# Kernel tuning notes

Hardware: AMD Instinct MI355X
Metric: run time of the kernel (lower is better)

The kernel has to match this reference:

```python
import jax, jax.numpy as jnp
import numpy as np

N, D, R, B, K = 16384, 300, 10, 1024, 64


def setup_inputs() -> dict:
    key = jax.random.key(0)
    ks = jax.random.split(key, 6)
    return {
        "node_feat_src": jax.random.normal(ks[0], (N, D), jnp.float32),
        "node_feat_tgt": jax.random.normal(ks[1], (N, D), jnp.float32),
        "srcs_index": jax.random.randint(ks[2], (B, K), 0, N),
        "tgts_index": jax.random.randint(ks[3], (B, K), 0, N),
        "src_vs": jax.random.normal(ks[4], (R, D), jnp.float32),
        "tgt_vs": jax.random.normal(ks[5], (R, D), jnp.float32),
    }


def _tower(h, vs):
    # Householder chain: h @ (I - v v^T / (v^T v)) == h - ((h v) / (v^T v)) v^T
    def step(h, v):
        coef = (h @ v) / (v @ v)  # [N]
        return h - coef[:, None] * v[None, :], None
    h, _ = jax.lax.scan(step, h, vs)
    return h


def _l2norm(x):
    # matches F.normalize(p=2, eps=1e-12) over the last dim
    n = jnp.linalg.norm(x, axis=-1, keepdims=True)
    return x / jnp.maximum(n, 1e-12)


def reference(node_feat_src, node_feat_tgt, srcs_index, tgts_index, src_vs, tgt_vs):
    src_h = _tower(node_feat_src, src_vs)  # [N, D]
    tgt_h = _tower(node_feat_tgt, tgt_vs)  # [N, D]

    pos_src = _l2norm(src_h[srcs_index[:, 0]])  # [B, D]
    pos_tgt = _l2norm(tgt_h[tgts_index[:, 0]])  # [B, D]
    src_list = _l2norm(src_h[srcs_index])       # [B, K, D]
    tgt_list = _l2norm(tgt_h[tgts_index])       # [B, K, D]

    sim_src2tgt = jnp.einsum('bd,bkd->bk', pos_src, tgt_list)  # [B, K]
    sim_tgt2src = jnp.einsum('bd,bkd->bk', pos_tgt, src_list)  # [B, K]

    # CSLS hubness penalties: mean of top-10 cross-domain cosine sims
    sim_matrix = _l2norm(src_h) @ _l2norm(tgt_h).T  # [N, N]
    rt = jnp.mean(jax.lax.top_k(sim_matrix, 10)[0], axis=1)    # [N]
    rs = jnp.mean(jax.lax.top_k(sim_matrix.T, 10)[0], axis=1)  # [N]

    srcs_rt = rt[srcs_index]  # [B, K]
    tgts_rs = rs[tgts_index]  # [B, K]

    logits_src2tgt = sim_src2tgt * 2 - srcs_rt[:, 0:1] - tgts_rs
    logits_tgt2src = sim_tgt2src * 2 - tgts_rs[:, 0:1] - srcs_rt
    return logits_src2tgt, logits_tgt2src
```

## Files before the change

kernel.cpp:

```cpp
#include <hip/hip_runtime.h>
#include <hip/hip_bf16.h>

#define NN 16384
#define DD 300
#define DP 320
#define RR 10
#define BB 1024
#define KK 64
#define CAP 128
#define CAPL 512

typedef __attribute__((ext_vector_type(8))) short s8v;
typedef __attribute__((ext_vector_type(4))) float f4v;
typedef _Float16 h2 __attribute__((ext_vector_type(2)));

__device__ __forceinline__ unsigned mono2(unsigned d) {
    unsigned s = ((d >> 15) & 0x10001u) * 0xFFFFu;
    return d ^ (s | 0x80008000u);
}
__device__ __forceinline__ float key2f16(unsigned k) {
    unsigned short b = (k & 0x8000u) ? (unsigned short)(k ^ 0x8000u)
                                     : (unsigned short)(~k & 0xFFFFu);
    _Float16 hv = __builtin_bit_cast(_Float16, b);
    return (float)hv;
}

__device__ __forceinline__ h2 h2max(h2 a, h2 b) {
    return __builtin_elementwise_max(a, b);
}
__device__ __forceinline__ h2 hmax2s(h2 a, int xb) {
    int x = __shfl_xor(__builtin_bit_cast(int, a), xb);
    return h2max(a, __builtin_bit_cast(h2, x));
}
__device__ __forceinline__ h2 packh2(float a, float b) {
    h2 r; r[0] = (_Float16)a; r[1] = (_Float16)b; return r;
}

__device__ __forceinline__ void ins10(unsigned (&lst)[10], unsigned v) {
    #pragma unroll
    for (int q = 0; q < 10; ++q) {
        unsigned a  = lst[q];
        unsigned mx = a > v ? a : v;
        v           = a > v ? v : a;
        lst[q] = mx;
    }
}
__device__ __forceinline__ void ins10f(float (&lst)[10], float v) {
    #pragma unroll
    for (int q = 0; q < 10; ++q) {
        float a  = lst[q];
        float mx = fmaxf(a, v);
        v        = fminf(a, v);
        lst[q] = mx;
    }
}

__device__ __forceinline__ void xcd_map(int bid, int& by, int& bx) {
    const int xcd = bid & 7;
    const int s   = bid >> 3;
    bx = (xcd << 2) | (s & 3);
    by = s >> 2;
}

__device__ __forceinline__ void gload_lds16(const void* g, void* l) {
#if __has_builtin(__builtin_amdgcn_global_load_lds)
    __builtin_amdgcn_global_load_lds(
        (const __attribute__((address_space(1))) void*)g,
        (__attribute__((address_space(3))) void*)l, 16, 0, 0);
#else
    const int lane = threadIdx.x & 63;
    int4 v = *reinterpret_cast<const int4*>(g);
    *reinterpret_cast<int4*>((char*)l + lane * 16) = v;
#endif
}

__device__ __forceinline__ void stage_tile(
        const __hip_bfloat16* __restrict__ Ab, const __hip_bfloat16* __restrict__ Bb,
        int kb, char* lds, int w, int lane) {
    const int r8 = lane >> 3;
    const int u  = (lane & 7) ^ r8;
    const int row = w * 8 + r8;
    const size_t go = (size_t)row * DP + kb * 64 + u * 8;
    gload_lds16(Ab + go, lds + w * 1024);
    gload_lds16(Bb + go, lds + 16384 + w * 1024);
}

__global__ __launch_bounds__(256) void tower_kernel(
        const float* __restrict__ feat, const float* __restrict__ vs,
        __hip_bfloat16* __restrict__ out) {
    __shared__ float vsh[RR * DD];
    const int tid = threadIdx.x;
    for (int i = tid; i < RR * DD; i += 256) vsh[i] = vs[i];
    __syncthreads();

    const int lane = tid & 63;
    const int wave = tid >> 6;
    const int row  = blockIdx.x * 4 + wave;

    float h[5];
    #pragma unroll
    for (int j = 0; j < 5; ++j) {
        int d = lane + 64 * j;
        h[j] = (d < DD) ? feat[(size_t)row * DD + d] : 0.f;
    }
    #pragma unroll
    for (int r = 0; r < RR; ++r) {
        float vl[5];
        float hv = 0.f, vv = 0.f;
        #pragma unroll
        for (int j = 0; j < 5; ++j) {
            int d = lane + 64 * j;
            float v = (d < DD) ? vsh[r * DD + d] : 0.f;
            vl[j] = v;
            hv += h[j] * v;
            vv += v * v;
        }
        #pragma unroll
        for (int o = 32; o; o >>= 1) {
            hv += __shfl_xor(hv, o);
            vv += __shfl_xor(vv, o);
        }
        float coef = hv / vv;
        #pragma unroll
        for (int j = 0; j < 5; ++j) h[j] -= coef * vl[j];
    }
    float nn = 0.f;
    #pragma unroll
    for (int j = 0; j < 5; ++j) nn += h[j] * h[j];
    #pragma unroll
    for (int o = 32; o; o >>= 1) nn += __shfl_xor(nn, o);
    float scale = 1.f / fmaxf(sqrtf(nn), 1e-12f);
    #pragma unroll
    for (int j = 0; j < 5; ++j) {
        int d = lane + 64 * j;
        float val = (d < DD) ? h[j] * scale : 0.f;
        out[(size_t)row * DP + d] = __float2bfloat16(val);
    }
}

__global__ __launch_bounds__(1024) void passA_kernel(
        const __hip_bfloat16* __restrict__ A, const __hip_bfloat16* __restrict__ Bm,
        unsigned short* __restrict__ rowsmax_g,
        unsigned short* __restrict__ colsmax_g) {
    __shared__ __align__(16) char u_lds[32768];
    __shared__ unsigned short rowsm[16][512];
    __shared__ unsigned short colsm[512][16];

    __hip_bfloat16* Asub = (__hip_bfloat16*)u_lds;
    __hip_bfloat16* Bsub = (__hip_bfloat16*)(u_lds + 16384);

    const int tid = threadIdx.x;
    const int lane = tid & 63;
    const int w = tid >> 6;
    const int wr = w >> 2, wc = w & 3;
    int by, bx; xcd_map(blockIdx.x, by, bx);
    const int i0 = by * 512, j0 = bx * 512;

    for (int ti = 0; ti < 4; ++ti) {
        for (int tj = 0; tj < 4; ++tj) {
            f4v acc[2][2];
            #pragma unroll
            for (int m = 0; m < 2; ++m)
                #pragma unroll
                for (int n = 0; n < 2; ++n)
                    acc[m][n] = (f4v){0.f, 0.f, 0.f, 0.f};

            const __hip_bfloat16* Ab = A  + (size_t)(i0 + ti * 128) * DP;
            const __hip_bfloat16* Bb = Bm + (size_t)(j0 + tj * 128) * DP;

            #pragma unroll
            for (int kb = 0; kb < 5; ++kb) {
                __syncthreads();
                stage_tile(Ab, Bb, kb, u_lds, w, lane);
                __syncthreads();
                #pragma unroll
                for (int ks = 0; ks < 2; ++ks) {
                    s8v af[2], bfv[2];
                    const int ulog = ks * 4 + (lane >> 4);
                    const int up   = ulog ^ (lane & 7);
                    #pragma unroll
                    for (int m = 0; m < 2; ++m) {
                        const int row = wr * 32 + m * 16 + (lane & 15);
                        af[m] = *reinterpret_cast<const s8v*>(Asub + row * 64 + up * 8);
                    }
                    #pragma unroll
                    for (int n = 0; n < 2; ++n) {
                        const int row = wc * 32 + n * 16 + (lane & 15);
                        bfv[n] = *reinterpret_cast<const s8v*>(Bsub + row * 64 + up * 8);
                    }
                    #pragma unroll
                    for (int m = 0; m < 2; ++m)
                        #pragma unroll
                        for (int n = 0; n < 2; ++n)
                            acc[m][n] = __builtin_amdgcn_mfma_f32_16x16x32_bf16(
                                af[m], bfv[n], acc[m][n], 0, 0, 0);
                }
            }

            #pragma unroll
            for (int m = 0; m < 2; ++m) {
                h2 a01 = h2max(packh2(acc[m][0][0], acc[m][0][1]),
                               packh2(acc[m][1][0], acc[m][1][1]));
                h2 a23 = h2max(packh2(acc[m][0][2], acc[m][0][3]),
                               packh2(acc[m][1][2], acc[m][1][3]));
                a01 = hmax2s(a01, 1); a23 = hmax2s(a23, 1);
                a01 = hmax2s(a01, 2); a23 = hmax2s(a23, 2);
                a01 = hmax2s(a01, 4); a23 = hmax2s(a23, 4);
                a01 = hmax2s(a01, 8); a23 = hmax2s(a23, 8);
                if ((lane & 15) == m * 8) {
                    const int rl = ti * 128 + wr * 32 + m * 16 + ((lane >> 4) << 2);
                    uint2 u = make_uint2(mono2(__builtin_bit_cast(unsigned, a01)),
                                         mono2(__builtin_bit_cast(unsigned, a23)));
                    *reinterpret_cast<uint2*>(&rowsm[tj * 4 + wc][rl]) = u;
                }
            }
            {
                float rm0 = -1e30f, rm1 = -1e30f;
                #pragma unroll
                for (int m = 0; m < 2; ++m) {
                    rm0 = fmaxf(rm0, fmaxf(fmaxf(acc[m][0][0], acc[m][0][1]),
                                           fmaxf(acc[m][0][2], acc[m][0][3])));
                    rm1 = fmaxf(rm1, fmaxf(fmaxf(acc[m][1][0], acc[m][1][1]),
                                           fmaxf(acc[m][1][2], acc[m][1][3])));
                }
                h2 c = packh2(rm0, rm1);
                c = hmax2s(c, 16);
                c = hmax2s(c, 32);
                if ((lane >> 4) == 0) {
                    const int s = ti * 4 + wr;
                    const int cb = tj * 128 + wc * 32 + (lane & 15);
                    unsigned k = mono2(__builtin_bit_cast(unsigned, c));
                    colsm[cb][s]      = (unsigned short)(k & 0xFFFFu);
                    colsm[cb + 16][s] = (unsigned short)(k >> 16);
                }
            }
        }
    }
    __syncthreads();
    if (tid < 512) {
        const int r = tid;
        unsigned short t16[16];
        #pragma unroll
        for (int s = 0; s < 16; ++s) t16[s] = rowsm[s][r];
        uint4 o0, o1;
        o0.x = t16[0] | ((unsigned)t16[1] << 16);  o0.y = t16[2] | ((unsigned)t16[3] << 16);
        o0.z = t16[4] | ((unsigned)t16[5] << 16);  o0.w = t16[6] | ((unsigned)t16[7] << 16);
        o1.x = t16[8] | ((unsigned)t16[9] << 16);  o1.y = t16[10] | ((unsigned)t16[11] << 16);
        o1.z = t16[12] | ((unsigned)t16[13] << 16); o1.w = t16[14] | ((unsigned)t16[15] << 16);
        uint4* rdst = reinterpret_cast<uint4*>(rowsmax_g + (size_t)(i0 + r) * 512 + bx * 16);
        rdst[0] = o0; rdst[1] = o1;
    } else {
        const int r = tid - 512;
        uint4 q0 = *reinterpret_cast<uint4*>(&colsm[r][0]);
        uint4 q1 = *reinterpret_cast<uint4*>(&colsm[r][8]);
        uint4* cdst = reinterpret_cast<uint4*>(colsmax_g + (size_t)(j0 + r) * 512 + by * 16);
        cdst[0] = q0; cdst[1] = q1;
    }
}

__global__ __launch_bounds__(256) void thresh_kernel(
        const unsigned short* __restrict__ rowsmax_g,
        const unsigned short* __restrict__ colsmax_g,
        float* __restrict__ Tlb_row, float* __restrict__ Tlb_col,
        unsigned* __restrict__ rowcnt, unsigned* __restrict__ colcnt) {
    const int t = blockIdx.x * 256 + threadIdx.x;
    const bool isRow = t < NN;
    const int idx = isRow ? t : t - NN;
    const unsigned short* src = (isRow ? rowsmax_g : colsmax_g) + (size_t)idx * 512;

    unsigned lst[10];
    #pragma unroll
    for (int q = 0; q < 10; ++q) lst[q] = 0u;

    const uint4* p = reinterpret_cast<const uint4*>(src);
    for (int c = 0; c < 64; ++c) {
        uint4 q = p[c];
        unsigned v0 = q.x & 0xFFFFu, v1 = q.x >> 16;
        unsigned v2 = q.y & 0xFFFFu, v3 = q.y >> 16;
        unsigned v4 = q.z & 0xFFFFu, v5 = q.z >> 16;
        unsigned v6 = q.w & 0xFFFFu, v7 = q.w >> 16;
        unsigned g01 = v0 > v1 ? v0 : v1, g23 = v2 > v3 ? v2 : v3;
        unsigned g45 = v4 > v5 ? v4 : v5, g67 = v6 > v7 ? v6 : v7;
        unsigned ga = g01 > g23 ? g01 : g23, gb = g45 > g67 ? g45 : g67;
        unsigned g = ga > gb ? ga : gb;
        if (g > lst[9]) {
            if (v0 > lst[9]) ins10(lst, v0);
            if (v1 > lst[9]) ins10(lst, v1);
            if (v2 > lst[9]) ins10(lst, v2);
            if (v3 > lst[9]) ins10(lst, v3);
            if (v4 > lst[9]) ins10(lst, v4);
            if (v5 > lst[9]) ins10(lst, v5);
            if (v6 > lst[9]) ins10(lst, v6);
            if (v7 > lst[9]) ins10(lst, v7);
        }
    }
    float f = key2f16(lst[9]);
    float lb = f - fabsf(f) * 0.002f - 1e-6f;
    if (isRow) { Tlb_row[idx] = lb; rowcnt[idx] = 0u; }
    else       { Tlb_col[idx] = lb; colcnt[idx] = 0u; }
}

__global__ __launch_bounds__(1024) void passB_kernel(
        const __hip_bfloat16* __restrict__ A, const __hip_bfloat16* __restrict__ Bm,
        const float* __restrict__ Tlb_row, const float* __restrict__ Tlb_col,
        unsigned* __restrict__ rowcnt, unsigned* __restrict__ colcnt,
        float* __restrict__ rowbuf, float* __restrict__ colbuf) {
    __shared__ __align__(16) char u_lds[32768];
    __shared__ float Trow_s[512];
    __shared__ float Tcol_s[512];
    __shared__ unsigned scnt[2];
    __shared__ uint2 sbuf[2][CAPL];

    __hip_bfloat16* Asub = (__hip_bfloat16*)u_lds;
    __hip_bfloat16* Bsub = (__hip_bfloat16*)(u_lds + 16384);

    const int tid = threadIdx.x;
    const int lane = tid & 63;
    const int w = tid >> 6;
    const int wr = w >> 2, wc = w & 3;
    int by, bx; xcd_map(blockIdx.x, by, bx);
    const int i0 = by * 512, j0 = bx * 512;

    if (tid < 512) Trow_s[tid] = Tlb_row[i0 + tid];
    else           Tcol_s[tid - 512] = Tlb_col[j0 + tid - 512];
    if (tid < 2) scnt[tid] = 0u;
    __syncthreads();

    for (int ti = 0; ti < 4; ++ti) {
        float trmin = 1e30f;
        #pragma unroll
        for (int m = 0; m < 2; ++m)
            #pragma unroll
            for (int r = 0; r < 4; ++r)
                trmin = fminf(trmin, Trow_s[ti * 128 + wr * 32 + m * 16 + ((lane >> 4) << 2) + r]);

        for (int tj = 0; tj < 4; ++tj) {
            f4v acc[2][2];
            #pragma unroll
            for (int m = 0; m < 2; ++m)
                #pragma unroll
                for (int n = 0; n < 2; ++n)
                    acc[m][n] = (f4v){0.f, 0.f, 0.f, 0.f};

            const __hip_bfloat16* Ab = A  + (size_t)(i0 + ti * 128) * DP;
            const __hip_bfloat16* Bb = Bm + (size_t)(j0 + tj * 128) * DP;

            #pragma unroll
            for (int kb = 0; kb < 5; ++kb) {
                __syncthreads();
                stage_tile(Ab, Bb, kb, u_lds, w, lane);
                __syncthreads();
                #pragma unroll
                for (int ks = 0; ks < 2; ++ks) {
                    s8v af[2], bfv[2];
                    const int ulog = ks * 4 + (lane >> 4);
                    const int up   = ulog ^ (lane & 7);
                    #pragma unroll
                    for (int m = 0; m < 2; ++m) {
                        const int row = wr * 32 + m * 16 + (lane & 15);
                        af[m] = *reinterpret_cast<const s8v*>(Asub + row * 64 + up * 8);
                    }
                    #pragma unroll
                    for (int n = 0; n < 2; ++n) {
                        const int row = wc * 32 + n * 16 + (lane & 15);
                        bfv[n] = *reinterpret_cast<const s8v*>(Bsub + row * 64 + up * 8);
                    }
                    #pragma unroll
                    for (int m = 0; m < 2; ++m)
                        #pragma unroll
                        for (int n = 0; n < 2; ++n)
                            acc[m][n] = __builtin_amdgcn_mfma_f32_16x16x32_bf16(
                                af[m], bfv[n], acc[m][n], 0, 0, 0);
                }
            }

            const int c0i = tj * 128 + wc * 32 + (lane & 15);
            const int c1i = c0i + 16;
            const float tc0 = Tcol_s[c0i], tc1 = Tcol_s[c1i];
            float vm = -1e30f;
            #pragma unroll
            for (int m = 0; m < 2; ++m) {
                float a = fmaxf(fmaxf(acc[m][0][0], acc[m][0][1]),
                                fmaxf(acc[m][0][2], acc[m][0][3]));
                float b = fmaxf(fmaxf(acc[m][1][0], acc[m][1][1]),
                                fmaxf(acc[m][1][2], acc[m][1][3]));
                vm = fmaxf(vm, fmaxf(a, b));
            }
            if (vm >= fminf(trmin, fminf(tc0, tc1))) {
                #pragma unroll
                for (int m = 0; m < 2; ++m) {
                    #pragma unroll
                    for (int r = 0; r < 4; ++r) {
                        const int rl = ti * 128 + wr * 32 + m * 16 + ((lane >> 4) << 2) + r;
                        const float T = Trow_s[rl];
                        const float v0 = acc[m][0][r], v1 = acc[m][1][r];
                        if (v0 >= T) {
                            unsigned p = atomicAdd(&scnt[0], 1u);
                            if (p < CAPL) sbuf[0][p] = make_uint2((unsigned)(i0 + rl), __float_as_uint(v0));
                            else { unsigned q = atomicAdd(&rowcnt[i0 + rl], 1u);
                                   if (q < CAP) rowbuf[(size_t)(i0 + rl) * CAP + q] = v0; }
                        }
                        if (v1 >= T) {
                            unsigned p = atomicAdd(&scnt[0], 1u);
                            if (p < CAPL) sbuf[0][p] = make_uint2((unsigned)(i0 + rl), __float_as_uint(v1));
                            else { unsigned q = atomicAdd(&rowcnt[i0 + rl], 1u);
                                   if (q < CAP) rowbuf[(size_t)(i0 + rl) * CAP + q] = v1; }
                        }
                        if (v0 >= tc0) {
                            unsigned p = atomicAdd(&scnt[1], 1u);
                            if (p < CAPL) sbuf[1][p] = make_uint2((unsigned)(j0 + c0i), __float_as_uint(v0));
                            else { unsigned q = atomicAdd(&colcnt[j0 + c0i], 1u);
                                   if (q < CAP) colbuf[(size_t)(j0 + c0i) * CAP + q] = v0; }
                        }
                        if (v1 >= tc1) {
                            unsigned p = atomicAdd(&scnt[1], 1u);
                            if (p < CAPL) sbuf[1][p] = make_uint2((unsigned)(j0 + c1i), __float_as_uint(v1));
                            else { unsigned q = atomicAdd(&colcnt[j0 + c1i], 1u);
                                   if (q < CAP) colbuf[(size_t)(j0 + c1i) * CAP + q] = v1; }
                        }
                    }
                }
            }
        }
    }

    __syncthreads();
    {
        const unsigned nr = scnt[0] < CAPL ? scnt[0] : CAPL;
        const unsigned nc = scnt[1] < CAPL ? scnt[1] : CAPL;
        for (unsigned i = tid; i < nr; i += 1024) {
            uint2 e = sbuf[0][i];
            unsigned p = atomicAdd(&rowcnt[e.x], 1u);
            if (p < CAP) rowbuf[(size_t)e.x * CAP + p] = __uint_as_float(e.y);
        }
        for (unsigned i = tid; i < nc; i += 1024) {
            uint2 e = sbuf[1][i];
            unsigned p = atomicAdd(&colcnt[e.x], 1u);
            if (p < CAP) colbuf[(size_t)e.x * CAP + p] = __uint_as_float(e.y);
        }
    }
}

__global__ __launch_bounds__(256) void final_kernel(
        const unsigned* __restrict__ rowcnt, const unsigned* __restrict__ colcnt,
        const float* __restrict__ rowbuf, const float* __restrict__ colbuf,
        float* __restrict__ rt, float* __restrict__ rs) {
    const int t = blockIdx.x * 256 + threadIdx.x;
    const bool isRow = t < NN;
    const int idx = isRow ? t : t - NN;
    const unsigned cn = (isRow ? rowcnt : colcnt)[idx];
    const int n = (int)(cn < CAP ? cn : CAP);
    const float* buf = (isRow ? rowbuf : colbuf) + (size_t)idx * CAP;

    float lst[10];
    #pragma unroll
    for (int q = 0; q < 10; ++q) lst[q] = -1e30f;
    for (int i = 0; i < n; ++i) {
        float v = buf[i];
        if (v > lst[9]) ins10f(lst, v);
    }
    float s = 0.f;
    #pragma unroll
    for (int q = 0; q < 10; ++q) s += lst[q];
    s *= 0.1f;
    (isRow ? rt : rs)[idx] = s;
}

__global__ __launch_bounds__(256) void logits_kernel(
        const __hip_bfloat16* __restrict__ srcH, const __hip_bfloat16* __restrict__ tgtH,
        const int* __restrict__ sidx, const int* __restrict__ tidx,
        const float* __restrict__ rt, const float* __restrict__ rs,
        float* __restrict__ out) {
    const int b    = blockIdx.x;
    const int lane = threadIdx.x & 63;
    const int w    = threadIdx.x >> 6;

    const int s0 = sidx[b * KK];
    const int t0 = tidx[b * KK];
    float ps[5], pt[5];
    #pragma unroll
    for (int j = 0; j < 5; ++j) {
        int d = lane + 64 * j;
        ps[j] = __bfloat162float(srcH[(size_t)s0 * DP + d]);
        pt[j] = __bfloat162float(tgtH[(size_t)t0 * DP + d]);
    }
    const float rt_s0 = rt[s0];
    const float rs_t0 = rs[t0];

    for (int kk = w; kk < KK; kk += 4) {
        const int it = tidx[b * KK + kk];
        const int is = sidx[b * KK + kk];
        float a = 0.f, c = 0.f;
        #pragma unroll
        for (int j = 0; j < 5; ++j) {
            int d = lane + 64 * j;
            a += ps[j] * __bfloat162float(tgtH[(size_t)it * DP + d]);
            c += pt[j] * __bfloat162float(srcH[(size_t)is * DP + d]);
        }
        #pragma unroll
        for (int o = 32; o; o >>= 1) {
            a += __shfl_xor(a, o);
            c += __shfl_xor(c, o);
        }
        if (lane == 0) {
            out[b * KK + kk]           = 2.f * a - rt_s0 - rs[it];
            out[BB * KK + b * KK + kk] = 2.f * c - rs_t0 - rt[is];
        }
    }
}

extern "C" void kernel_launch(void* const* d_in, const int* in_sizes, int n_in,
                              void* d_out, int out_size, void* d_ws, size_t ws_size,
                              hipStream_t stream) {
    const float* nf_src = (const float*)d_in[0];
    const float* nf_tgt = (const float*)d_in[1];
    const int*   sidx   = (const int*)d_in[2];
    const int*   tidx   = (const int*)d_in[3];
    const float* svs    = (const float*)d_in[4];
    const float* tvs    = (const float*)d_in[5];

    char* ws = (char*)d_ws;
    const size_t SZ_H  = (size_t)NN * DP * 2;
    const size_t SZ_SM = (size_t)NN * 512 * 2;
    __hip_bfloat16* srcH = (__hip_bfloat16*)ws;
    __hip_bfloat16* tgtH = (__hip_bfloat16*)(ws + SZ_H);
    unsigned short* rowsmax = (unsigned short*)(ws + 2 * SZ_H);
    unsigned short* colsmax = (unsigned short*)(ws + 2 * SZ_H + SZ_SM);
    float* rowbuf = (float*)(ws + 2 * SZ_H);
    float* colbuf = (float*)(ws + 2 * SZ_H + (size_t)NN * CAP * 4);
    char* tail = ws + 2 * SZ_H + 2 * SZ_SM;
    float* Tlb_row = (float*)(tail);
    float* Tlb_col = (float*)(tail + 65536);
    unsigned* rowcnt = (unsigned*)(tail + 2 * 65536);
    unsigned* colcnt = (unsigned*)(tail + 3 * 65536);
    float* rt = (float*)(tail + 4 * 65536);
    float* rs = (float*)(tail + 5 * 65536);

    tower_kernel<<<NN / 4, 256, 0, stream>>>(nf_src, svs, srcH);
    tower_kernel<<<NN / 4, 256, 0, stream>>>(nf_tgt, tvs, tgtH);
    passA_kernel<<<1024, 1024, 0, stream>>>(srcH, tgtH, rowsmax, colsmax);
    thresh_kernel<<<(2 * NN) / 256, 256, 0, stream>>>(rowsmax, colsmax, Tlb_row, Tlb_col,
                                                      rowcnt, colcnt);
    passB_kernel<<<1024, 1024, 0, stream>>>(srcH, tgtH, Tlb_row, Tlb_col,
                                            rowcnt, colcnt, rowbuf, colbuf);
    final_kernel<<<(2 * NN) / 256, 256, 0, stream>>>(rowcnt, colcnt, rowbuf, colbuf, rt, rs);
    logits_kernel<<<BB, 256, 0, stream>>>(srcH, tgtH, sidx, tidx, rt, rs, (float*)d_out);
}
```

Baseline: 738.5 us.

## Double-buffer LDS tiles with async global-to-LDS prefetch in GEMM passes

Both similarity GEMM passes now use two LDS buffers. The next k-block is loaded directly into LDS while the current one is computed, with explicit vmcnt waits and raw s_barrier replacing the two __syncthreads per k-step. The aim is to hide global-load latency behind the MFMA work. LDS per block doubles to 64KB for the staging buffer, which may lower occupancy, and correctness now rests on hand-placed waitcnt and barriers.

```diff
diff --git a/kernel.cpp b/kernel.cpp
--- a/kernel.cpp
+++ b/kernel.cpp
@@ -76,13 +76,13 @@
 
 __device__ __forceinline__ void stage_tile(
         const __hip_bfloat16* __restrict__ Ab, const __hip_bfloat16* __restrict__ Bb,
-        int kb, char* lds, int w, int lane) {
+        int kb, char* base, int w, int lane) {
     const int r8 = lane >> 3;
     const int u  = (lane & 7) ^ r8;
     const int row = w * 8 + r8;
     const size_t go = (size_t)row * DP + kb * 64 + u * 8;
-    gload_lds16(Ab + go, lds + w * 1024);
-    gload_lds16(Bb + go, lds + 16384 + w * 1024);
+    gload_lds16(Ab + go, base + w * 1024);
+    gload_lds16(Bb + go, base + 16384 + w * 1024);
 }
 
 __global__ __launch_bounds__(256) void tower_kernel(
@@ -138,16 +138,57 @@
     }
 }
 
+#define KLOOP(COMPUTE_BODY)                                                    \
+    stage_tile(Ab, Bb, 0, u_lds, w, lane);                                     \
+    _Pragma("unroll")                                                          \
+    for (int kb = 0; kb < 5; ++kb) {                                           \
+        char* curb = u_lds + (kb & 1) * 32768;                                 \
+        if (kb < 4)                                                            \
+            stage_tile(Ab, Bb, kb + 1, u_lds + ((kb + 1) & 1) * 32768, w, lane); \
+        if (kb < 4) { asm volatile("s_waitcnt vmcnt(2)" ::: "memory"); }       \
+        else        { asm volatile("s_waitcnt vmcnt(0)" ::: "memory"); }       \
+        __builtin_amdgcn_s_barrier();                                          \
+        asm volatile("" ::: "memory");                                         \
+        {                                                                      \
+            const __hip_bfloat16* Asub = (const __hip_bfloat16*)curb;          \
+            const __hip_bfloat16* Bsub = (const __hip_bfloat16*)(curb + 16384);\
+            COMPUTE_BODY                                                       \
+        }                                                                      \
+        asm volatile("" ::: "memory");                                         \
+        __builtin_amdgcn_s_barrier();                                          \
+    }
+
+#define COMPUTE_TILE                                                           \
+    _Pragma("unroll")                                                          \
+    for (int ks = 0; ks < 2; ++ks) {                                           \
+        s8v af[2], bfv[2];                                                     \
+        const int ulog = ks * 4 + (lane >> 4);                                 \
+        const int up   = ulog ^ (lane & 7);                                    \
+        _Pragma("unroll")                                                      \
+        for (int m = 0; m < 2; ++m) {                                          \
+            const int row = wr * 32 + m * 16 + (lane & 15);                    \
+            af[m] = *reinterpret_cast<const s8v*>(Asub + row * 64 + up * 8);   \
+        }                                                                      \
+        _Pragma("unroll")                                                      \
+        for (int n = 0; n < 2; ++n) {                                          \
+            const int row = wc * 32 + n * 16 + (lane & 15);                    \
+            bfv[n] = *reinterpret_cast<const s8v*>(Bsub + row * 64 + up * 8);  \
+        }                                                                      \
+        _Pragma("unroll")                                                      \
+        for (int m = 0; m < 2; ++m)                                            \
+            _Pragma("unroll")                                                  \
+            for (int n = 0; n < 2; ++n)                                        \
+                acc[m][n] = __builtin_amdgcn_mfma_f32_16x16x32_bf16(           \
+                    af[m], bfv[n], acc[m][n], 0, 0, 0);                        \
+    }
+
 __global__ __launch_bounds__(1024) void passA_kernel(
         const __hip_bfloat16* __restrict__ A, const __hip_bfloat16* __restrict__ Bm,
         unsigned short* __restrict__ rowsmax_g,
         unsigned short* __restrict__ colsmax_g) {
-    __shared__ __align__(16) char u_lds[32768];
+    __shared__ __align__(16) char u_lds[65536];
     __shared__ unsigned short rowsm[16][512];
     __shared__ unsigned short colsm[512][16];
-
-    __hip_bfloat16* Asub = (__hip_bfloat16*)u_lds;
-    __hip_bfloat16* Bsub = (__hip_bfloat16*)(u_lds + 16384);
 
     const int tid = threadIdx.x;
     const int lane = tid & 63;
@@ -168,34 +209,7 @@
             const __hip_bfloat16* Ab = A  + (size_t)(i0 + ti * 128) * DP;
             const __hip_bfloat16* Bb = Bm + (size_t)(j0 + tj * 128) * DP;
 
-            #pragma unroll
-            for (int kb = 0; kb < 5; ++kb) {
-                __syncthreads();
-                stage_tile(Ab, Bb, kb, u_lds, w, lane);
-                __syncthreads();
-                #pragma unroll
-                for (int ks = 0; ks < 2; ++ks) {
-                    s8v af[2], bfv[2];
-                    const int ulog = ks * 4 + (lane >> 4);
-                    const int up   = ulog ^ (lane & 7);
-                    #pragma unroll
-                    for (int m = 0; m < 2; ++m) {
-                        const int row = wr * 32 + m * 16 + (lane & 15);
-                        af[m] = *reinterpret_cast<const s8v*>(Asub + row * 64 + up * 8);
-                    }
-                    #pragma unroll
-                    for (int n = 0; n < 2; ++n) {
-                        const int row = wc * 32 + n * 16 + (lane & 15);
-                        bfv[n] = *reinterpret_cast<const s8v*>(Bsub + row * 64 + up * 8);
-                    }
-                    #pragma unroll
-                    for (int m = 0; m < 2; ++m)
-                        #pragma unroll
-                        for (int n = 0; n < 2; ++n)
-                            acc[m][n] = __builtin_amdgcn_mfma_f32_16x16x32_bf16(
-                                af[m], bfv[n], acc[m][n], 0, 0, 0);
-                }
-            }
+            KLOOP(COMPUTE_TILE)
 
             #pragma unroll
             for (int m = 0; m < 2; ++m) {
@@ -305,14 +319,11 @@
         const float* __restrict__ Tlb_row, const float* __restrict__ Tlb_col,
         unsigned* __restrict__ rowcnt, unsigned* __restrict__ colcnt,
         float* __restrict__ rowbuf, float* __restrict__ colbuf) {
-    __shared__ __align__(16) char u_lds[32768];
+    __shared__ __align__(16) char u_lds[65536];
     __shared__ float Trow_s[512];
     __shared__ float Tcol_s[512];
     __shared__ unsigned scnt[2];
     __shared__ uint2 sbuf[2][CAPL];
-
-    __hip_bfloat16* Asub = (__hip_bfloat16*)u_lds;
-    __hip_bfloat16* Bsub = (__hip_bfloat16*)(u_lds + 16384);
 
     const int tid = threadIdx.x;
     const int lane = tid & 63;
@@ -345,34 +356,7 @@
             const __hip_bfloat16* Ab = A  + (size_t)(i0 + ti * 128) * DP;
             const __hip_bfloat16* Bb = Bm + (size_t)(j0 + tj * 128) * DP;
 
-            #pragma unroll
-            for (int kb = 0; kb < 5; ++kb) {
-                __syncthreads();
-                stage_tile(Ab, Bb, kb, u_lds, w, lane);
-                __syncthreads();
-                #pragma unroll
-                for (int ks = 0; ks < 2; ++ks) {
-                    s8v af[2], bfv[2];
-                    const int ulog = ks * 4 + (lane >> 4);
-                    const int up   = ulog ^ (lane & 7);
-                    #pragma unroll
-                    for (int m = 0; m < 2; ++m) {
-                        const int row = wr * 32 + m * 16 + (lane & 15);
-                        af[m] = *reinterpret_cast<const s8v*>(Asub + row * 64 + up * 8);
-                    }
-                    #pragma unroll
-                    for (int n = 0; n < 2; ++n) {
-                        const int row = wc * 32 + n * 16 + (lane & 15);
-                        bfv[n] = *reinterpret_cast<const s8v*>(Bsub + row * 64 + up * 8);
-                    }
-                    #pragma unroll
-                    for (int m = 0; m < 2; ++m)
-                        #pragma unroll
-                        for (int n = 0; n < 2; ++n)
-                            acc[m][n] = __builtin_amdgcn_mfma_f32_16x16x32_bf16(
-                                af[m], bfv[n], acc[m][n], 0, 0, 0);
-                }
-            }
+            KLOOP(COMPUTE_TILE)
 
             const int c0i = tj * 128 + wc * 32 + (lane & 15);
             const int c1i = c0i + 16;
```

After: 632.8 us (median of 2 runs). 14.3% less time.
